# Kernel tuning notes

Hardware: AMD Instinct MI355X
Metric: run time of the kernel (lower is better)

## Reference

```python
import jax, jax.numpy as jnp
import numpy as np

B, S, E, H, DH = 256, 256, 384, 6, 64
NEG_INF = -1e9


def setup_inputs() -> dict:
    key = jax.random.key(0)
    ks = jax.random.split(key, 8)
    sc = 0.02
    return {
        "x": jax.random.normal(ks[0], (B, S, E), jnp.float32),
        "Wq": jax.random.normal(ks[1], (H, E, DH), jnp.float32) * sc,
        "Wk": jax.random.normal(ks[2], (H, E, DH), jnp.float32) * sc,
        "Wv": jax.random.normal(ks[3], (H, E, DH), jnp.float32) * sc,
        "Wp": jax.random.normal(ks[4], (E, E), jnp.float32) * sc,
        "bp": jnp.zeros((E,), jnp.float32),
        "W1": jax.random.normal(ks[5], (E, 4 * E), jnp.float32) * sc,
        "b1": jnp.zeros((4 * E,), jnp.float32),
        "W2": jax.random.normal(ks[6], (4 * E, E), jnp.float32) * sc,
        "b2": jnp.zeros((E,), jnp.float32),
        "g1": jnp.ones((E,), jnp.float32),
        "be1": jnp.zeros((E,), jnp.float32),
        "g2": jnp.ones((E,), jnp.float32),
        "be2": jnp.zeros((E,), jnp.float32),
    }


def _layernorm(x, g, b, eps=1e-5):
    mu = jnp.mean(x, axis=-1, keepdims=True)
    var = jnp.mean(jnp.square(x - mu), axis=-1, keepdims=True)
    return (x - mu) * jax.lax.rsqrt(var + eps) * g + b


def reference(x, Wq, Wk, Wv, Wp, bp, W1, b1, W2, b2, g1, be1, g2, be2):
    # --- pre-attention LayerNorm ---
    h = _layernorm(x, g1, be1)
    # --- multi-head causal self-attention (all heads vectorized) ---
    q = jnp.einsum('bse,hed->bhsd', h, Wq)
    k = jnp.einsum('bse,hed->bhsd', h, Wk)
    v = jnp.einsum('bse,hed->bhsd', h, Wv)
    scores = jnp.einsum('bhsd,bhtd->bhst', q, k) * (DH ** -0.5)
    causal = jnp.tril(jnp.ones((S, S), dtype=bool))
    scores = jnp.where(causal, scores, NEG_INF)
    att = jax.nn.softmax(scores, axis=-1)  # dropout = identity at eval
    o = jnp.einsum('bhst,bhtd->bhsd', att, v)
    o = o.transpose(0, 2, 1, 3).reshape(x.shape[0], S, E)  # concat heads
    x = x + (o @ Wp + bp)
    # --- FFN block ---
    h2 = _layernorm(x, g2, be2)
    ffn = jax.nn.relu(h2 @ W1 + b1) @ W2 + b2
    return x + ffn
```

## Files before the change

### kernel.cpp

```cpp
#include <hip/hip_runtime.h>
#include <hip/hip_bf16.h>
#include <stdint.h>

typedef __bf16 bf16_t;
typedef __bf16 bf16x2 __attribute__((ext_vector_type(2)));
typedef __bf16 bf16x8 __attribute__((ext_vector_type(8)));
typedef float f32x4 __attribute__((ext_vector_type(4)));

#define NB 256
#define NS 256
#define NE 384
#define NH 6
#define ND 64
#define NM (NB*NS)

__device__ __forceinline__ f32x4 mfma16(bf16x8 a, bf16x8 b, f32x4 c) {
    return __builtin_amdgcn_mfma_f32_16x16x32_bf16(a, b, c, 0, 0, 0);
}

__device__ __forceinline__ void cp16_async(const bf16_t* g, const bf16_t* l) {
    __builtin_amdgcn_global_load_lds(
        (__attribute__((address_space(1))) void*)g,
        (__attribute__((address_space(3))) void*)l, 16, 0, 0);
}

__global__ void wqkv_trans(const float* __restrict__ Wq, const float* __restrict__ Wk,
                           const float* __restrict__ Wv, bf16_t* __restrict__ Wcat)
{
    int i = blockIdx.x * 256 + threadIdx.x;
    if (i >= NH*NE*ND) return;
    int d = i & 63;
    int e = (i >> 6) % NE;
    int h = i / (NE*ND);
    int n = h*64 + d;
    Wcat[(size_t)(0*NE*NH*ND) + (size_t)n*NE + e]            = (bf16_t)Wq[i];
    Wcat[(size_t)(NE)*(NH*ND) + (size_t)(384 + n)*NE + e - (size_t)(NE)*(NH*ND)] = (bf16_t)Wk[i];
    Wcat[(size_t)(768 + n)*NE + e]                            = (bf16_t)Wv[i];
}

__global__ void wtrans(const float* __restrict__ src, bf16_t* __restrict__ dst, int K, int N)
{
    int i = blockIdx.x * 256 + threadIdx.x;
    if (i >= K*N) return;
    int k = i / N, n = i % N;
    dst[(size_t)n*K + k] = (bf16_t)src[i];
}

__global__ __launch_bounds__(256) void ln_kernel(
    const float* __restrict__ x, const float* __restrict__ g,
    const float* __restrict__ be, bf16_t* __restrict__ o)
{
    const int wave = threadIdx.x >> 6, lane = threadIdx.x & 63;
    const int row = blockIdx.x * 4 + wave;
    const float* xr = x + (size_t)row * NE;
    float v[6]; float s = 0.f, sq = 0.f;
    #pragma unroll
    for (int i = 0; i < 6; i++) { v[i] = xr[i*64 + lane]; s += v[i]; sq += v[i]*v[i]; }
    #pragma unroll
    for (int off = 32; off > 0; off >>= 1) { s += __shfl_xor(s, off); sq += __shfl_xor(sq, off); }
    const float mean = s * (1.f/NE);
    const float rstd = rsqrtf(sq * (1.f/NE) - mean*mean + 1e-5f);
    bf16_t* orow = o + (size_t)row * NE;
    #pragma unroll
    for (int i = 0; i < 6; i++) {
        int e = i*64 + lane;
        orow[e] = (bf16_t)((v[i] - mean) * rstd * g[e] + be[e]);
    }
}

template<int OUT_MODE, bool RELU>
__global__ __launch_bounds__(256, 2) void gemm_bt(
    const bf16_t* __restrict__ A, const bf16_t* __restrict__ Bt,
    void* __restrict__ outp, const float* __restrict__ bias,
    const float* __restrict__ res, int M, int N, int K, int ldb)
{
    __shared__ bf16_t sA[2][128*32];
    __shared__ bf16_t sB[2][128*32];
    const int tid = threadIdx.x;
    const int wave = tid >> 6, lane = tid & 63;
    const int l15 = lane & 15, quad = lane >> 4;
    const int m0 = blockIdx.x * 128;
    const int n0 = blockIdx.y * 128;
    const int wm = wave >> 1, wn = wave & 1;

    const int srow = lane >> 2;
    const int scol = (lane & 3) * 8;
    const bf16_t* gA = A  + (size_t)(m0 + 32*wave + srow) * K + scol;
    const bf16_t* gB = Bt + (size_t)(n0 + 32*wave + srow) * ldb + scol;

    const f32x4 zero = {0.f, 0.f, 0.f, 0.f};
    f32x4 acc[4][4];
    #pragma unroll
    for (int a = 0; a < 4; a++)
        #pragma unroll
        for (int b = 0; b < 4; b++) acc[a][b] = zero;

    const int nk = K >> 5;
    cp16_async(gA, &sA[0][(32*wave)*32]);
    cp16_async(gA + (size_t)16*K, &sA[0][(32*wave + 16)*32]);
    cp16_async(gB, &sB[0][(32*wave)*32]);
    cp16_async(gB + (size_t)16*ldb, &sB[0][(32*wave + 16)*32]);

    for (int it = 0; it < nk; it++) {
        __syncthreads();
        if (it + 1 < nk) {
            int kt = (it + 1) << 5;
            int nb = (it + 1) & 1;
            cp16_async(gA + kt, &sA[nb][(32*wave)*32]);
            cp16_async(gA + (size_t)16*K + kt, &sA[nb][(32*wave + 16)*32]);
            cp16_async(gB + kt, &sB[nb][(32*wave)*32]);
            cp16_async(gB + (size_t)16*ldb + kt, &sB[nb][(32*wave + 16)*32]);
        }
        const int cb = it & 1;
        bf16x8 af[4], bfr[4];
        #pragma unroll
        for (int i = 0; i < 4; i++)
            af[i] = *(const bf16x8*)&sA[cb][(64*wm + 16*i + l15)*32 + quad*8];
        #pragma unroll
        for (int i = 0; i < 4; i++)
            bfr[i] = *(const bf16x8*)&sB[cb][(64*wn + 16*i + l15)*32 + quad*8];
        #pragma unroll
        for (int mi = 0; mi < 4; mi++)
            #pragma unroll
            for (int ni = 0; ni < 4; ni++)
                acc[mi][ni] = mfma16(af[mi], bfr[ni], acc[mi][ni]);
    }

    #pragma unroll
    for (int mi = 0; mi < 4; mi++) {
        #pragma unroll
        for (int ni = 0; ni < 4; ni++) {
            #pragma unroll
            for (int r = 0; r < 4; r++) {
                int gm = m0 + 64*wm + 16*mi + quad*4 + r;
                int gn = n0 + 64*wn + 16*ni + l15;
                float v = acc[mi][ni][r];
                if (bias) v += bias[gn];
                if (res)  v += res[(size_t)gm*N + gn];
                if (RELU) v = fmaxf(v, 0.f);
                if (OUT_MODE == 1) {
                    int sel = (gn >= 768) ? 2 : ((gn >= 384) ? 1 : 0);
                    int within = gn - sel*384;
                    int b = gm >> 8, s = gm & 255, h = within >> 6, d = within & 63;
                    ((bf16_t*)outp)[(size_t)sel*((size_t)NM*384) +
                                    (((size_t)b*NH + h)*NS + s)*ND + d] = (bf16_t)v;
                } else if (OUT_MODE == 2) {
                    ((float*)outp)[(size_t)gm*N + gn] = v;
                } else {
                    ((bf16_t*)outp)[(size_t)gm*N + gn] = (bf16_t)v;
                }
            }
        }
    }
}

__global__ __launch_bounds__(256) void attn_kernel(
    const bf16_t* __restrict__ Qg, const bf16_t* __restrict__ Kg,
    const bf16_t* __restrict__ Vg, bf16_t* __restrict__ Og)
{
    __shared__ bf16_t sK[256*72];
    __shared__ bf16_t sVT[64*264];
    __shared__ bf16_t sQ[64*72];
    __shared__ bf16_t sS[64*264];
    __shared__ float sMax[64*4];
    __shared__ float sSum[64*4];
    __shared__ float sRowSum[64];

    const int tid = threadIdx.x;
    const int wave = tid >> 6, lane = tid & 63;
    const int l15 = lane & 15, quad = lane >> 4;
    const int bh = blockIdx.x;
    const int b = bh / NH, h = bh % NH;
    const size_t base = (size_t)bh * (NS*ND);
    const bf16_t* Qb = Qg + base;
    const bf16_t* Kb = Kg + base;
    const bf16_t* Vb = Vg + base;

    #pragma unroll
    for (int it = 0; it < 8; it++) {
        int idx = it*256 + tid;
        int t = idx >> 3, c = idx & 7;
        bf16x8 kv = *(const bf16x8*)(Kb + t*64 + c*8);
        *(bf16x8*)&sK[t*72 + c*8] = kv;
        bf16x8 vv = *(const bf16x8*)(Vb + t*64 + c*8);
        #pragma unroll
        for (int j = 0; j < 8; j++) sVT[(c*8 + j)*264 + t] = vv[j];
    }

    const int r = lane;
    const int p = wave;
    const f32x4 zero = {0.f, 0.f, 0.f, 0.f};

    for (int mt = 0; mt < 4; mt++) {
        __syncthreads();
        #pragma unroll
        for (int it = 0; it < 2; it++) {
            int idx = it*256 + tid;
            int qr = idx >> 3, c = idx & 7;
            *(bf16x8*)&sQ[qr*72 + c*8] = *(const bf16x8*)(Qb + (64*mt + qr)*64 + c*8);
        }
        __syncthreads();
        if (wave <= mt) {
            const int ct = wave;
            bf16x8 bk[2][4];
            #pragma unroll
            for (int ks = 0; ks < 2; ks++)
                #pragma unroll
                for (int ni = 0; ni < 4; ni++)
                    bk[ks][ni] = *(const bf16x8*)&sK[(64*ct + 16*ni + l15)*72 + ks*32 + quad*8];
            #pragma unroll
            for (int mi = 0; mi < 4; mi++) {
                bf16x8 a0 = *(const bf16x8*)&sQ[(16*mi + l15)*72 + quad*8];
                bf16x8 a1 = *(const bf16x8*)&sQ[(16*mi + l15)*72 + 32 + quad*8];
                f32x4 sc[4];
                #pragma unroll
                for (int ni = 0; ni < 4; ni++) sc[ni] = zero;
                #pragma unroll
                for (int ni = 0; ni < 4; ni++) sc[ni] = mfma16(a0, bk[0][ni], sc[ni]);
                #pragma unroll
                for (int ni = 0; ni < 4; ni++) sc[ni] = mfma16(a1, bk[1][ni], sc[ni]);
                #pragma unroll
                for (int ni = 0; ni < 4; ni++)
                    #pragma unroll
                    for (int rr = 0; rr < 4; rr++)
                        sS[(16*mi + quad*4 + rr)*264 + 64*ct + 16*ni + l15] =
                            (bf16_t)(sc[ni][rr] * 0.125f);
            }
        }
        __syncthreads();
        const int sg = 64*mt + r;
        float mx = -INFINITY;
        if (p <= mt) {
            #pragma unroll
            for (int c = 0; c < 8; c++) {
                bf16x8 v8 = *(const bf16x8*)&sS[r*264 + 64*p + c*8];
                #pragma unroll
                for (int j = 0; j < 8; j++) {
                    int t = 64*p + c*8 + j;
                    float v = (float)v8[j];
                    mx = (t <= sg) ? fmaxf(mx, v) : mx;
                }
            }
        }
        sMax[r*4 + p] = mx;
        __syncthreads();
        const float rmax = fmaxf(fmaxf(sMax[r*4+0], sMax[r*4+1]),
                                 fmaxf(sMax[r*4+2], sMax[r*4+3]));
        float sum = 0.f;
        if (p <= mt) {
            #pragma unroll
            for (int c = 0; c < 8; c++) {
                bf16x8 v8 = *(const bf16x8*)&sS[r*264 + 64*p + c*8];
                bf16x8 e8;
                #pragma unroll
                for (int j = 0; j < 8; j++) {
                    int t = 64*p + c*8 + j;
                    float e = 0.f;
                    if (t <= sg) e = __expf((float)v8[j] - rmax);
                    sum += e;
                    e8[j] = (bf16_t)e;
                }
                *(bf16x8*)&sS[r*264 + 64*p + c*8] = e8;
            }
        }
        sSum[r*4 + p] = sum;
        __syncthreads();
        if (p == 0) sRowSum[r] = sSum[r*4+0] + sSum[r*4+1] + sSum[r*4+2] + sSum[r*4+3];
        __syncthreads();
        f32x4 oacc[4];
        #pragma unroll
        for (int ni = 0; ni < 4; ni++) oacc[ni] = zero;
        for (int kt = 0; kt <= mt; kt++) {
            bf16x8 a = *(const bf16x8*)&sS[(16*p + l15)*264 + 64*kt + quad*8];
            #pragma unroll
            for (int ni = 0; ni < 4; ni++) {
                bf16x8 bv = *(const bf16x8*)&sVT[(16*ni + l15)*264 + 64*kt + quad*8];
                oacc[ni] = mfma16(a, bv, oacc[ni]);
            }
        }
        #pragma unroll
        for (int ni = 0; ni < 4; ni++) {
            #pragma unroll
            for (int rr = 0; rr < 4; rr++) {
                int lrow = 16*p + quad*4 + rr;
                float inv = 1.0f / sRowSum[lrow];
                int srow_g = 64*mt + lrow;
                int d = 16*ni + l15;
                Og[((size_t)(b*NS + srow_g))*NE + h*ND + d] = (bf16_t)(oacc[ni][rr] * inv);
            }
        }
    }
}

extern "C" void kernel_launch(void* const* d_in, const int* in_sizes, int n_in,
                              void* d_out, int out_size, void* d_ws, size_t ws_size,
                              hipStream_t stream)
{
    (void)in_sizes; (void)n_in; (void)out_size; (void)ws_size;
    const float* x   = (const float*)d_in[0];
    const float* Wq  = (const float*)d_in[1];
    const float* Wk  = (const float*)d_in[2];
    const float* Wv  = (const float*)d_in[3];
    const float* Wp  = (const float*)d_in[4];
    const float* bp  = (const float*)d_in[5];
    const float* W1  = (const float*)d_in[6];
    const float* b1  = (const float*)d_in[7];
    const float* W2  = (const float*)d_in[8];
    const float* b2  = (const float*)d_in[9];
    const float* g1  = (const float*)d_in[10];
    const float* be1 = (const float*)d_in[11];
    const float* g2  = (const float*)d_in[12];
    const float* be2 = (const float*)d_in[13];
    float* out = (float*)d_out;

    char* ws = (char*)d_ws;
    const size_t SZ = (size_t)NM * NE * 2;
    bf16_t* h_bf  = (bf16_t*)(ws);
    bf16_t* q_bf  = (bf16_t*)(ws + SZ);
    bf16_t* k_bf  = (bf16_t*)(ws + 2*SZ);
    bf16_t* v_bf  = (bf16_t*)(ws + 3*SZ);
    bf16_t* o_bf  = (bf16_t*)(ws);
    bf16_t* h2_bf = (bf16_t*)(ws);
    bf16_t* hid   = (bf16_t*)(ws + SZ);
    char* wb = ws + 4*SZ;
    bf16_t* Wcat = (bf16_t*)(wb);
    bf16_t* Wpt  = (bf16_t*)(wb + 884736);
    bf16_t* W1t  = (bf16_t*)(wb + 884736 + 294912);
    bf16_t* W2t  = (bf16_t*)(wb + 884736 + 294912 + 1179648);

    wqkv_trans<<<(NH*NE*ND + 255)/256, 256, 0, stream>>>(Wq, Wk, Wv, Wcat);
    wtrans<<<(NE*NE + 255)/256, 256, 0, stream>>>(Wp, Wpt, NE, NE);
    wtrans<<<(NE*4*NE + 255)/256, 256, 0, stream>>>(W1, W1t, NE, 4*NE);
    wtrans<<<(NE*4*NE + 255)/256, 256, 0, stream>>>(W2, W2t, 4*NE, NE);

    ln_kernel<<<NM/4, 256, 0, stream>>>(x, g1, be1, h_bf);

    dim3 gqkv(NM/128, 9), g384(NM/128, 3), gffn(NM/128, 6);
    gemm_bt<1,false><<<gqkv, 256, 0, stream>>>(h_bf, Wcat, q_bf, nullptr, nullptr, NM, 1152, NE, NE);

    attn_kernel<<<NB*NH, 256, 0, stream>>>(q_bf, k_bf, v_bf, o_bf);

    gemm_bt<2,false><<<g384, 256, 0, stream>>>(o_bf, Wpt, out, bp, x, NM, NE, NE, NE);

    ln_kernel<<<NM/4, 256, 0, stream>>>(out, g2, be2, h2_bf);

    gemm_bt<3,true ><<<gffn, 256, 0, stream>>>(h2_bf, W1t, hid, b1, nullptr, NM, 768, NE, NE);
    gemm_bt<2,false><<<g384, 256, 0, stream>>>(hid, W2t, out, b2, out, NM, NE, 768, 1536);

    gemm_bt<3,true ><<<gffn, 256, 0, stream>>>(h2_bf, W1t + (size_t)768*NE, hid, b1 + 768, nullptr, NM, 768, NE, NE);
    gemm_bt<2,false><<<g384, 256, 0, stream>>>(hid, W2t + 768, out, nullptr, out, NM, NE, 768, 1536);
}
```

Before: 1.005 ms.

## Triple-buffer GEMM shared-memory tiles with explicit vmcnt waits

Moves the bf16 GEMM main loop from a double buffer to a three-slot ring of shared-memory tiles, prefetching two K-steps ahead. Synchronisation now uses explicit s_waitcnt vmcnt counts plus raw s_barrier in place of __syncthreads, so the loop only waits for the oldest outstanding async copy. Launch bounds are raised to three blocks per CU. The goal is to hide global-load latency behind MFMA work, at the cost of 50% more LDS per block and register pressure under the tighter launch bound. Correctness depends on the hand-counted vmcnt values matching the number of async loads issued.

Result: no change. 1.015 ms (+1.0%).

```diff
diff --git a/kernel.cpp b/kernel.cpp
--- a/kernel.cpp
+++ b/kernel.cpp
@@ -69,13 +69,13 @@
 }
 
 template<int OUT_MODE, bool RELU>
-__global__ __launch_bounds__(256, 2) void gemm_bt(
+__global__ __launch_bounds__(256, 3) void gemm_bt(
     const bf16_t* __restrict__ A, const bf16_t* __restrict__ Bt,
     void* __restrict__ outp, const float* __restrict__ bias,
     const float* __restrict__ res, int M, int N, int K, int ldb)
 {
-    __shared__ bf16_t sA[2][128*32];
-    __shared__ bf16_t sB[2][128*32];
+    __shared__ bf16_t sA[3][128*32];
+    __shared__ bf16_t sB[3][128*32];
     const int tid = threadIdx.x;
     const int wave = tid >> 6, lane = tid & 63;
     const int l15 = lane & 15, quad = lane >> 4;
@@ -96,22 +96,31 @@
         for (int b = 0; b < 4; b++) acc[a][b] = zero;
 
     const int nk = K >> 5;
-    cp16_async(gA, &sA[0][(32*wave)*32]);
-    cp16_async(gA + (size_t)16*K, &sA[0][(32*wave + 16)*32]);
-    cp16_async(gB, &sB[0][(32*wave)*32]);
-    cp16_async(gB + (size_t)16*ldb, &sB[0][(32*wave + 16)*32]);
-
-    for (int it = 0; it < nk; it++) {
-        __syncthreads();
-        if (it + 1 < nk) {
-            int kt = (it + 1) << 5;
-            int nb = (it + 1) & 1;
-            cp16_async(gA + kt, &sA[nb][(32*wave)*32]);
-            cp16_async(gA + (size_t)16*K + kt, &sA[nb][(32*wave + 16)*32]);
-            cp16_async(gB + kt, &sB[nb][(32*wave)*32]);
-            cp16_async(gB + (size_t)16*ldb + kt, &sB[nb][(32*wave + 16)*32]);
-        }
-        const int cb = it & 1;
+
+    auto issue = [&](int t, int slot) {
+        const int kt = t << 5;
+        cp16_async(gA + kt,                 &sA[slot][(32*wave)*32]);
+        cp16_async(gA + (size_t)16*K + kt,  &sA[slot][(32*wave + 16)*32]);
+        cp16_async(gB + kt,                 &sB[slot][(32*wave)*32]);
+        cp16_async(gB + (size_t)16*ldb + kt,&sB[slot][(32*wave + 16)*32]);
+    };
+
+    issue(0, 0);
+    issue(1, 1);
+
+    int cb = 0;
+    int ns = 2;
+    for (int it = 0; it < nk; ++it) {
+        asm volatile("s_barrier" ::: "memory");
+        if (it + 2 < nk) {
+            issue(it + 2, ns);
+            asm volatile("s_waitcnt vmcnt(8)\n\ts_barrier" ::: "memory");
+        } else if (it + 1 < nk) {
+            asm volatile("s_waitcnt vmcnt(4)\n\ts_barrier" ::: "memory");
+        } else {
+            asm volatile("s_waitcnt vmcnt(0)\n\ts_barrier" ::: "memory");
+        }
+
         bf16x8 af[4], bfr[4];
         #pragma unroll
         for (int i = 0; i < 4; i++)
@@ -124,6 +133,9 @@
             #pragma unroll
             for (int ni = 0; ni < 4; ni++)
                 acc[mi][ni] = mfma16(af[mi], bfr[ni], acc[mi][ni]);
+
+        cb = (cb == 2) ? 0 : cb + 1;
+        ns = (ns == 2) ? 0 : ns + 1;
     }
 
     #pragma unroll
```
